# Kernel optimization log

Measured on AMD Instinct MI355X. Metric: run time of the kernel, lower is better.

## Reference

```python
import jax, jax.numpy as jnp
import numpy as np

B, N, T = 64, 1024, 512  # batch, node_num (= input_dim = hidden_dim), seq_len


def setup_inputs() -> dict:
    key = jax.random.key(0)
    k0, k1, k2, k3, k4 = jax.random.split(key, 5)
    flow_x = jax.random.normal(k0, (B, N, T, 1), dtype=jnp.float32)
    s = 1.0 / np.sqrt(N)  # torch nn.Linear default init bound
    W1 = jax.random.uniform(k1, (N, 2 * N), jnp.float32, -s, s)
    b1 = jax.random.uniform(k2, (2 * N,), jnp.float32, -s, s)
    W2 = jax.random.uniform(k3, (N, N), jnp.float32, -s, s)
    b2 = jax.random.uniform(k4, (N,), jnp.float32, -s, s)
    return {"flow_x": flow_x, "W1": W1, "b1": b1, "W2": W2, "b2": b2}


def reference(flow_x, W1, b1, W2, b2):
    Bs, Nn, Ts, _ = flow_x.shape
    # [B, N, T, 1] -> [B, T, N]
    x = jnp.transpose(flow_x, (0, 2, 1, 3)).reshape(Bs, Ts, Nn)
    # Precompute input projections for all timesteps (batched GEMM)
    xp = x @ W1 + b1                      # [B, T, 2N]
    xh = x @ W2 + b2                      # [B, T, N]
    x1, x2 = jnp.split(xp, 2, axis=-1)    # each [B, T, N]

    def step(h, inp):
        x1t, x2t, xht = inp               # each [B, N]
        hp = h @ W1 + b1                  # [B, 2N]
        h1, h2 = jnp.split(hp, 2, axis=-1)
        z = jax.nn.sigmoid(x1t + h1)
        r = jax.nn.sigmoid(x2t + h2)
        h_hat = jnp.tanh(xht + r * (h @ W2 + b2))
        h_new = z * h + (1.0 - z) * h_hat
        return h_new, None

    h0 = jnp.zeros((Bs, Nn), dtype=x.dtype)
    xs = (jnp.swapaxes(x1, 0, 1), jnp.swapaxes(x2, 0, 1), jnp.swapaxes(xh, 0, 1))
    hT, _ = jax.lax.scan(step, h0, xs)
    # original returns last output reshaped to [B, N, 1, 1]
    return hT.reshape(Bs, Nn, 1, 1)
```

## Files before the change

### kernel.cpp

```cpp
#include <hip/hip_runtime.h>


#define BATCH 64
#define NN 1024
#define TSTEPS 512
#define HB_ELEMS ((size_t)BATCH * NN)

typedef __attribute__((ext_vector_type(8))) short short8;
typedef __attribute__((ext_vector_type(8))) unsigned short u16x8;
typedef __attribute__((ext_vector_type(4))) unsigned short u16x4;
typedef __attribute__((ext_vector_type(4))) float f32x4;

#define MFMA16(a, b, c) __builtin_amdgcn_mfma_f32_16x16x32_bf16((a), (b), (c), 0, 0, 0)

__device__ __forceinline__ unsigned short f2bf(float x) {
  union { float f; unsigned u; } v; v.f = x;
  unsigned u = v.u + 0x7FFFu + ((v.u >> 16) & 1u);
  return (unsigned short)(u >> 16);
}
__device__ __forceinline__ float bf2f(unsigned short h) {
  union { unsigned u; float f; } v; v.u = ((unsigned)h) << 16; return v.f;
}

__global__ void trans_x(const float* __restrict__ fx, unsigned short* __restrict__ xT) {
  int bid = blockIdx.x;
  int b   = bid >> 7;
  int rem = bid & 127;
  int kt  = rem >> 3;
  int tt  = rem & 7;
  __shared__ float tl[64][65];
  int tx = threadIdx.x & 63;
  int ty = threadIdx.x >> 6;
  const float* src = fx + ((size_t)(b * NN + kt * 64)) * TSTEPS + tt * 64;
#pragma unroll
  for (int i = 0; i < 16; i++) {
    int kr = i * 4 + ty;
    tl[kr][tx] = src[(size_t)kr * TSTEPS + tx];
  }
  __syncthreads();
#pragma unroll
  for (int i = 0; i < 16; i++) {
    int tr = i * 4 + ty;
    xT[((size_t)((tt * 64 + tr) * 64 + b)) * NN + kt * 64 + tx] = f2bf(tl[tx][tr]);
  }
}

__global__ void prep_w(const float* __restrict__ W1, const float* __restrict__ W2,
                       unsigned short* __restrict__ wt) {
  int bid = blockIdx.x;
  int s    = bid >> 8;
  int tile = bid & 255;
  int kt = tile >> 4, jt = tile & 15;
  const float* src = (s < 2) ? W1 : W2;
  int ld = (s < 2) ? 2048 : 1024;
  int co = (s == 1) ? 1024 : 0;
  __shared__ float tl[64][65];
  int tx = threadIdx.x & 63, ty = threadIdx.x >> 6;
#pragma unroll
  for (int i = 0; i < 16; i++) {
    int kr = i * 4 + ty;
    tl[kr][tx] = src[(size_t)(kt * 64 + kr) * ld + co + jt * 64 + tx];
  }
  __syncthreads();
#pragma unroll
  for (int i = 0; i < 16; i++) {
    int jr = i * 4 + ty;
    wt[((size_t)(s * NN + jt * 64 + jr)) * NN + kt * 64 + tx] = f2bf(tl[tx][jr]);
  }
}

__global__ __launch_bounds__(256) void precompute(
    const unsigned short* __restrict__ xT, const unsigned short* __restrict__ wt,
    const float* __restrict__ b1, const float* __restrict__ b2,
    unsigned short* __restrict__ P2) {
  int m0 = (blockIdx.x / 24) * 128;
  int n0 = (blockIdx.x % 24) * 128;
  __shared__ unsigned short As[128 * 40];
  __shared__ unsigned short Bs[128 * 40];
  int tid = threadIdx.x;
  int wave = tid >> 6, lane = tid & 63, q = lane >> 4, li = lane & 15;
  int wm = wave >> 1, wn = wave & 1;
  f32x4 acc[4][4];
#pragma unroll
  for (int a = 0; a < 4; a++)
#pragma unroll
    for (int b = 0; b < 4; b++) acc[a][b] = (f32x4)(0.f);

  for (int kk = 0; kk < 32; ++kk) {
    int K0 = kk * 32;
#pragma unroll
    for (int e = 0; e < 2; e++) {
      int c = tid * 2 + e;
      int row = c >> 2, part = c & 3;
      *(u16x8*)&As[row * 40 + part * 8] =
          *(const u16x8*)&xT[(size_t)(m0 + row) * NN + K0 + part * 8];
      *(u16x8*)&Bs[row * 40 + part * 8] =
          *(const u16x8*)&wt[(size_t)(n0 + row) * NN + K0 + part * 8];
    }
    __syncthreads();
    short8 af[4], bfr[4];
#pragma unroll
    for (int mt = 0; mt < 4; mt++)
      af[mt] = *(const short8*)&As[(wm * 64 + mt * 16 + li) * 40 + q * 8];
#pragma unroll
    for (int nt = 0; nt < 4; nt++)
      bfr[nt] = *(const short8*)&Bs[(wn * 64 + nt * 16 + li) * 40 + q * 8];
#pragma unroll
    for (int mt = 0; mt < 4; mt++)
#pragma unroll
      for (int nt = 0; nt < 4; nt++)
        acc[mt][nt] = MFMA16(af[mt], bfr[nt], acc[mt][nt]);
    __syncthreads();
  }
#pragma unroll
  for (int mt = 0; mt < 4; mt++) {
    int m = m0 + wm * 64 + mt * 16 + q * 4;
    int t = m >> 6, b = m & 63;
#pragma unroll
    for (int nt = 0; nt < 4; nt++) {
      int n = n0 + wn * 64 + nt * 16 + li;
      float bias = (n < 2048) ? b1[n] : b2[n - 2048];
      int s = n >> 10, j = n & 1023;
      f32x4 a = acc[mt][nt];
      u16x4 pk;
      pk.x = f2bf(a.x + bias); pk.y = f2bf(a.y + bias);
      pk.z = f2bf(a.z + bias); pk.w = f2bf(a.w + bias);
      *(u16x4*)&P2[(((size_t)t * 3 + s) * NN + j) * 64 + b] = pk;
    }
  }
}

#define AL(p)    __hip_atomic_load((p),  __ATOMIC_RELAXED, __HIP_MEMORY_SCOPE_AGENT)
#define AS(p, v) __hip_atomic_store((p), (v), __ATOMIC_RELAXED, __HIP_MEMORY_SCOPE_AGENT)

__global__ __launch_bounds__(256, 1) void gru_scan(
    unsigned short* __restrict__ hb, const unsigned short* __restrict__ wt,
    const unsigned short* __restrict__ P2,
    const float* __restrict__ b1, const float* __restrict__ b2,
    float* __restrict__ out, unsigned* __restrict__ cnt) {
  int bid = blockIdx.x;
  int jt = bid & 63, mq = bid >> 6;
  int j0 = jt * 16, m0 = mq * 16;
  int tid = threadIdx.x, wave = tid >> 6, lane = tid & 63, q = lane >> 4, li = lane & 15;
  int kb = wave * 256;

  const short8* Bz = (const short8*)&wt[((size_t)(0 * NN + j0 + li)) * NN + kb + q * 8];
  const short8* Br = (const short8*)&wt[((size_t)(1 * NN + j0 + li)) * NN + kb + q * 8];
  const short8* Bv = (const short8*)&wt[((size_t)(2 * NN + j0 + li)) * NN + kb + q * 8];
  short8 wz[8], wr[8], wv[8];
#pragma unroll
  for (int r = 0; r < 8; r++) {
    wz[r] = Bz[r * 4];
    wr[r] = Br[r * 4];
    wv[r] = Bv[r * 4];
  }

  int j = j0 + li;
  int bbase = m0 + q * 4;
  float b1z = b1[j], b1r = b1[NN + j], b2v = b2[j];
  const unsigned short* pz = &P2[((size_t)0 * NN + j) * 64 + bbase];
  const unsigned short* pr = &P2[((size_t)1 * NN + j) * 64 + bbase];
  const unsigned short* pv = &P2[((size_t)2 * NN + j) * 64 + bbase];
  const size_t pstride = (size_t)3 * NN * 64;

  unsigned* poll_w = &cnt[(mq * 4 + wave) * 64];
  unsigned* arr_w  = &cnt[(mq * 4 + (jt >> 4)) * 64];

  const size_t aoff = (size_t)(m0 + li) * 256 + wave * 64 + q * 2;

  f32x4 hc = (f32x4)(0.f);
  __shared__ f32x4 red[9][64];

  for (int t = 0; t < TSTEPS; t++) {
    u16x4 pz4, pr4, pv4;
    if (wave == 0) {
      pz4 = *(const u16x4*)pz;
      pr4 = *(const u16x4*)pr;
      pv4 = *(const u16x4*)pv;
    }
    if (t > 0) {
      unsigned target = 16u * (unsigned)t;
      while (AL(poll_w) < target) __builtin_amdgcn_s_sleep(1);
    }
    const unsigned long long* hin =
        (const unsigned long long*)(hb + ((size_t)(t & 3)) * HB_ELEMS);
    union { unsigned long long u[2]; short8 s; } fa[8];
#pragma unroll
    for (int r = 0; r < 8; r++) {
      fa[r].u[0] = AL(hin + aoff + r * 8);
      fa[r].u[1] = AL(hin + aoff + r * 8 + 1);
    }
    f32x4 az = (f32x4)(0.f), ar = (f32x4)(0.f), av = (f32x4)(0.f);
#pragma unroll
    for (int r = 0; r < 8; r++) {
      az = MFMA16(fa[r].s, wz[r], az);
      ar = MFMA16(fa[r].s, wr[r], ar);
      av = MFMA16(fa[r].s, wv[r], av);
    }
    if (wave > 0) {
      red[(wave - 1) * 3 + 0][lane] = az;
      red[(wave - 1) * 3 + 1][lane] = ar;
      red[(wave - 1) * 3 + 2][lane] = av;
    }
    __syncthreads();
    if (wave == 0) {
#pragma unroll
      for (int w = 0; w < 3; w++) {
        az += red[w * 3 + 0][lane];
        ar += red[w * 3 + 1][lane];
        av += red[w * 3 + 2][lane];
      }
#pragma unroll
      for (int reg = 0; reg < 4; reg++) {
        float z = 1.f / (1.f + __expf(-(az[reg] + bf2f(pz4[reg]) + b1z)));
        float r = 1.f / (1.f + __expf(-(ar[reg] + bf2f(pr4[reg]) + b1r)));
        float x = bf2f(pv4[reg]) + r * (av[reg] + b2v);
        float e = __expf(-2.f * fabsf(x));
        float th = (1.f - e) / (1.f + e);
        float hh = (x >= 0.f) ? th : -th;
        hc[reg] = z * hc[reg] + (1.f - z) * hh;
      }
      if (t < TSTEPS - 1) {
        unsigned* hout = (unsigned*)(hb + ((size_t)((t + 1) & 3)) * HB_ELEMS);
#pragma unroll
        for (int reg = 0; reg < 4; reg++) {
          unsigned mine = f2bf(hc[reg]);
          unsigned other = (unsigned)__shfl_xor((int)mine, 1, 64);
          if ((lane & 1) == 0) {
            unsigned packed = mine | (other << 16);
            AS(&hout[(size_t)(bbase + reg) * (NN / 2) + (j >> 1)], packed);
          }
        }
        asm volatile("s_waitcnt vmcnt(0)" ::: "memory");
        if (lane == 0)
          __hip_atomic_fetch_add(arr_w, 1u, __ATOMIC_RELAXED,
                                 __HIP_MEMORY_SCOPE_AGENT);
      }
    }
    pz += pstride; pr += pstride; pv += pstride;
  }

  if (wave == 0) {
#pragma unroll
    for (int reg = 0; reg < 4; reg++)
      out[(size_t)(bbase + reg) * NN + j] = hc[reg];
  }
}

extern "C" void kernel_launch(void* const* d_in, const int* in_sizes, int n_in,
                              void* d_out, int out_size, void* d_ws, size_t ws_size,
                              hipStream_t stream) {
  const float* flow_x = (const float*)d_in[0];
  const float* W1 = (const float*)d_in[1];
  const float* b1 = (const float*)d_in[2];
  const float* W2 = (const float*)d_in[3];
  const float* b2 = (const float*)d_in[4];
  float* out = (float*)d_out;
  char* ws = (char*)d_ws;
  size_t off = 0;
  auto take = [&](size_t bytes) -> char* {
    char* p = ws + off;
    off += (bytes + 255) & ~(size_t)255;
    return p;
  };
  unsigned short* wt  = (unsigned short*)take((size_t)3 * 1024 * 1024 * 2);
  unsigned short* xT  = (unsigned short*)take((size_t)32768 * 1024 * 2);
  unsigned short* P2  = (unsigned short*)take((size_t)512 * 3 * 1024 * 64 * 2);
  unsigned short* hb  = (unsigned short*)take((size_t)4 * HB_ELEMS * 2);
  unsigned*       cnt = (unsigned*)take((size_t)16 * 64 * 4);

  if (off > ws_size) {
    hipMemsetAsync(d_out, 0, (size_t)out_size * 4, stream);
    return;
  }

  hipMemsetAsync(hb, 0, HB_ELEMS * 2, stream);
  hipMemsetAsync(cnt, 0, (size_t)16 * 64 * 4, stream);

  prep_w<<<768, 256, 0, stream>>>(W1, W2, wt);
  trans_x<<<8192, 256, 0, stream>>>(flow_x, xT);
  precompute<<<6144, 256, 0, stream>>>(xT, wt, b1, b2, P2);

  void* args[] = {&hb, &wt, &P2, &b1, &b2, &out, &cnt};
  hipLaunchCooperativeKernel((const void*)gru_scan, dim3(256), dim3(256),
                             args, 0, stream);
}
```

Measured before the change: 3.584 ms.

## Replace atomic arrival counters with per-block step flags polled across lanes

The inter-block barrier used to have each producer block atomically increment a shared counter that consumer waves polled. Now each block stores its step number to its own flag, and a consumer wave has its 16 lanes each poll one producer flag, combined with a wave-wide all-vote. This removes contention on the atomic read-modify-write. The shared reduction buffer is double-buffered by step parity so one step's LDS writes cannot clobber the previous step's reads. A spin cap breaks out of the wait after a fixed number of iterations, which risks reading stale hidden state if a producer is slow.

```diff
diff --git a/kernel.cpp b/kernel.cpp
--- a/kernel.cpp
+++ b/kernel.cpp
@@ -5,6 +5,7 @@
 #define NN 1024
 #define TSTEPS 512
 #define HB_ELEMS ((size_t)BATCH * NN)
+#define SPIN_CAP 16384
 
 typedef __attribute__((ext_vector_type(8))) short short8;
 typedef __attribute__((ext_vector_type(8))) unsigned short u16x8;
@@ -137,7 +138,7 @@
     unsigned short* __restrict__ hb, const unsigned short* __restrict__ wt,
     const unsigned short* __restrict__ P2,
     const float* __restrict__ b1, const float* __restrict__ b2,
-    float* __restrict__ out, unsigned* __restrict__ cnt) {
+    float* __restrict__ out, unsigned* __restrict__ flags) {
   int bid = blockIdx.x;
   int jt = bid & 63, mq = bid >> 6;
   int j0 = jt * 16, m0 = mq * 16;
@@ -163,13 +164,13 @@
   const unsigned short* pv = &P2[((size_t)2 * NN + j) * 64 + bbase];
   const size_t pstride = (size_t)3 * NN * 64;
 
-  unsigned* poll_w = &cnt[(mq * 4 + wave) * 64];
-  unsigned* arr_w  = &cnt[(mq * 4 + (jt >> 4)) * 64];
+  unsigned* myflag = &flags[(mq * 4 + (jt >> 4)) * 64 + (jt & 15)];
+  const unsigned* pollp = &flags[(mq * 4 + wave) * 64 + li];
 
   const size_t aoff = (size_t)(m0 + li) * 256 + wave * 64 + q * 2;
 
   f32x4 hc = (f32x4)(0.f);
-  __shared__ f32x4 red[9][64];
+  __shared__ f32x4 red[2][9][64];
 
   for (int t = 0; t < TSTEPS; t++) {
     u16x4 pz4, pr4, pv4;
@@ -179,8 +180,12 @@
       pv4 = *(const u16x4*)pv;
     }
     if (t > 0) {
-      unsigned target = 16u * (unsigned)t;
-      while (AL(poll_w) < target) __builtin_amdgcn_s_sleep(1);
+      unsigned tgt = (unsigned)t;
+      int spins = 0;
+      while (!__all((int)(AL(pollp) >= tgt))) {
+        if (++spins > SPIN_CAP) break;
+        __builtin_amdgcn_s_sleep(1);
+      }
     }
     const unsigned long long* hin =
         (const unsigned long long*)(hb + ((size_t)(t & 3)) * HB_ELEMS);
@@ -197,18 +202,19 @@
       ar = MFMA16(fa[r].s, wr[r], ar);
       av = MFMA16(fa[r].s, wv[r], av);
     }
+    f32x4* rp = &red[t & 1][0][0];
     if (wave > 0) {
-      red[(wave - 1) * 3 + 0][lane] = az;
-      red[(wave - 1) * 3 + 1][lane] = ar;
-      red[(wave - 1) * 3 + 2][lane] = av;
+      rp[((wave - 1) * 3 + 0) * 64 + lane] = az;
+      rp[((wave - 1) * 3 + 1) * 64 + lane] = ar;
+      rp[((wave - 1) * 3 + 2) * 64 + lane] = av;
     }
     __syncthreads();
     if (wave == 0) {
 #pragma unroll
       for (int w = 0; w < 3; w++) {
-        az += red[w * 3 + 0][lane];
-        ar += red[w * 3 + 1][lane];
-        av += red[w * 3 + 2][lane];
+        az += rp[(w * 3 + 0) * 64 + lane];
+        ar += rp[(w * 3 + 1) * 64 + lane];
+        av += rp[(w * 3 + 2) * 64 + lane];
       }
 #pragma unroll
       for (int reg = 0; reg < 4; reg++) {
@@ -232,9 +238,7 @@
           }
         }
         asm volatile("s_waitcnt vmcnt(0)" ::: "memory");
-        if (lane == 0)
-          __hip_atomic_fetch_add(arr_w, 1u, __ATOMIC_RELAXED,
-                                 __HIP_MEMORY_SCOPE_AGENT);
+        if (lane == 0) AS(myflag, (unsigned)(t + 1));
       }
     }
     pz += pstride; pr += pstride; pv += pstride;
@@ -263,11 +267,11 @@
     off += (bytes + 255) & ~(size_t)255;
     return p;
   };
-  unsigned short* wt  = (unsigned short*)take((size_t)3 * 1024 * 1024 * 2);
-  unsigned short* xT  = (unsigned short*)take((size_t)32768 * 1024 * 2);
-  unsigned short* P2  = (unsigned short*)take((size_t)512 * 3 * 1024 * 64 * 2);
-  unsigned short* hb  = (unsigned short*)take((size_t)4 * HB_ELEMS * 2);
-  unsigned*       cnt = (unsigned*)take((size_t)16 * 64 * 4);
+  unsigned short* wt    = (unsigned short*)take((size_t)3 * 1024 * 1024 * 2);
+  unsigned short* xT    = (unsigned short*)take((size_t)32768 * 1024 * 2);
+  unsigned short* P2    = (unsigned short*)take((size_t)512 * 3 * 1024 * 64 * 2);
+  unsigned short* hb    = (unsigned short*)take((size_t)4 * HB_ELEMS * 2);
+  unsigned*       flags = (unsigned*)take((size_t)16 * 64 * 4);
 
   if (off > ws_size) {
     hipMemsetAsync(d_out, 0, (size_t)out_size * 4, stream);
@@ -275,13 +279,13 @@
   }
 
   hipMemsetAsync(hb, 0, HB_ELEMS * 2, stream);
-  hipMemsetAsync(cnt, 0, (size_t)16 * 64 * 4, stream);
+  hipMemsetAsync(flags, 0, (size_t)16 * 64 * 4, stream);
 
   prep_w<<<768, 256, 0, stream>>>(W1, W2, wt);
   trans_x<<<8192, 256, 0, stream>>>(flow_x, xT);
   precompute<<<6144, 256, 0, stream>>>(xT, wt, b1, b2, P2);
 
-  void* args[] = {&hb, &wt, &P2, &b1, &b2, &out, &cnt};
+  void* args[] = {&hb, &wt, &P2, &b1, &b2, &out, &flags};
   hipLaunchCooperativeKernel((const void*)gru_scan, dim3(256), dim3(256),
                              args, 0, stream);
 }
```

Result: faster. 3.419 ms (-4.6%).
